# Optimization experiments

Hardware: AMD Instinct MI355X
Metric: run time of the kernel (lower is better)

The kernel has to match this reference:

```python
import jax, jax.numpy as jnp
import numpy as np

D_MODEL = 1024
N_HEADS = 16
D_HEAD = D_MODEL // N_HEADS
BSZ, SEQ = 1, 4096


def setup_inputs() -> dict:
    key = jax.random.key(0)
    ks = jax.random.split(key, 7)
    scale = 1.0 / np.sqrt(D_MODEL)
    q = jax.random.normal(ks[0], (BSZ, SEQ, D_MODEL), dtype=jnp.float32)
    k = jax.random.normal(ks[1], (BSZ, SEQ, D_MODEL), dtype=jnp.float32)
    v = jax.random.normal(ks[2], (BSZ, SEQ, D_MODEL), dtype=jnp.float32)
    Wq = jax.random.normal(ks[3], (D_MODEL, D_MODEL), dtype=jnp.float32) * scale
    Wk = jax.random.normal(ks[4], (D_MODEL, D_MODEL), dtype=jnp.float32) * scale
    Wv = jax.random.normal(ks[5], (D_MODEL, D_MODEL), dtype=jnp.float32) * scale
    Wo = jax.random.normal(ks[6], (D_MODEL, D_MODEL), dtype=jnp.float32) * scale
    # causal mask: 1 = attend, 0 = masked (matches torch masked_fill(mask == 0, -inf))
    mask = jnp.tril(jnp.ones((SEQ, SEQ), dtype=jnp.int32))[None, None, :, :]
    return {"q": q, "k": k, "v": v, "mask": mask, "Wq": Wq, "Wk": Wk, "Wv": Wv, "Wo": Wo}


def reference(q, k, v, mask, Wq, Wk, Wv, Wo):
    bsz, seq, _ = q.shape
    # nn.Linear(d,d,bias=False): y = x @ W.T
    Q = (q @ Wq.T).reshape(bsz, seq, N_HEADS, D_HEAD).transpose(0, 2, 1, 3)
    K = (k @ Wk.T).reshape(bsz, seq, N_HEADS, D_HEAD).transpose(0, 2, 1, 3)
    V = (v @ Wv.T).reshape(bsz, seq, N_HEADS, D_HEAD).transpose(0, 2, 1, 3)
    scores = jnp.einsum("bhqd,bhkd->bhqk", Q, K) / np.sqrt(D_HEAD).astype(np.float32)
    scores = jnp.where(mask == 0, -jnp.inf, scores)
    attn = jax.nn.softmax(scores, axis=-1)
    out = jnp.einsum("bhqk,bhkd->bhqd", attn, V)
    out = out.transpose(0, 2, 1, 3).reshape(bsz, seq, D_MODEL)
    return out @ Wo.T
```

## Files before the change

### kernel.cpp

```cpp
#include <hip/hip_runtime.h>


typedef __attribute__((ext_vector_type(8))) short bf16x8;
typedef __attribute__((ext_vector_type(4))) float f32x4;
typedef __attribute__((ext_vector_type(16))) float f32x16;

#define S_LEN 4096
#define DM 1024
#define NH 16
#define DH 64

static __device__ __forceinline__ unsigned short f2bf(float f) {
  union { float f; unsigned u; } x; x.f = f;
  unsigned u = x.u;
  u += 0x7fffu + ((u >> 16) & 1u);
  return (unsigned short)(u >> 16);
}

static __device__ __forceinline__ unsigned pk2(float lo, float hi) {
  unsigned r;
  asm("v_cvt_pk_bf16_f32 %0, %1, %2" : "=v"(r) : "v"(lo), "v"(hi));
  return r;
}

static __device__ __forceinline__ void swap32u(unsigned& a, unsigned& b) {
  asm("v_permlane32_swap_b32 %0, %1" : "+v"(a), "+v"(b));
}

static __device__ __forceinline__ float exp2_(float x) {
#if __has_builtin(__builtin_amdgcn_exp2f)
  return __builtin_amdgcn_exp2f(x);
#else
  return exp2f(x);
#endif
}

#define GLL16(gsrc, ldst)                                                      \
  __builtin_amdgcn_global_load_lds(                                            \
      (const __attribute__((address_space(1))) void*)(gsrc),                   \
      (__attribute__((address_space(3))) void*)(ldst), 16, 0, 0)

struct CastArgs {
  const float* src[8];
  unsigned short* dst[8];
  int n[8];
  float scl[8];
};

__global__ __launch_bounds__(256) void cast_all(CastArgs a) {
  int which = blockIdx.y;
  const float* __restrict__ src = a.src[which];
  unsigned short* __restrict__ dst = a.dst[which];
  int n = a.n[which];
  float s = a.scl[which];
  int i = (blockIdx.x * 256 + threadIdx.x) * 8;
  if (i >= n) return;
  f32x4 v0 = *(const f32x4*)(src + i);
  f32x4 v1 = *(const f32x4*)(src + i + 4);
  union { bf16x8 v; unsigned short u[8]; } o;
#pragma unroll
  for (int j = 0; j < 4; j++) { o.u[j] = f2bf(v0[j] * s); o.u[4 + j] = f2bf(v1[j] * s); }
  *(bf16x8*)(dst + i) = o.v;
}

static __device__ __forceinline__ void gemm_body(
    const unsigned short* __restrict__ A, const unsigned short* __restrict__ B,
    void* __restrict__ Cout, int mode, unsigned short* As, unsigned short* Bs) {
  const int K = 1024;
  int tid = threadIdx.x;
  int wid = tid >> 6, lane = tid & 63;
  int m0 = blockIdx.y * 128, n0 = blockIdx.x * 128;
  int wr = (wid >> 1) * 64, wc = (wid & 1) * 64;
  int g = lane >> 4, r = lane & 15;

  const int srow = wid * 8 + (lane >> 3);
  const int scol = 8 * ((lane & 7) ^ ((lane >> 3) & 7));
  const unsigned short* gA[4];
  const unsigned short* gB[4];
#pragma unroll
  for (int rr = 0; rr < 4; rr++) {
    gA[rr] = A + (size_t)(m0 + rr * 32 + srow) * K + scol;
    gB[rr] = B + (size_t)(n0 + rr * 32 + srow) * K + scol;
  }

  f32x4 acc[4][4] = {};
  const int rsw = (r & 7) << 3;

  for (int k0 = 0; k0 < K; k0 += 64) {
#pragma unroll
    for (int rr = 0; rr < 4; rr++) {
      GLL16(gA[rr] + k0, As + wid * 512 + rr * 2048);
      GLL16(gB[rr] + k0, Bs + wid * 512 + rr * 2048);
    }
    __syncthreads();

#pragma unroll
    for (int kk = 0; kk < 64; kk += 32) {
      bf16x8 af[4], bfr[4];
#pragma unroll
      for (int mi = 0; mi < 4; mi++)
        af[mi] = *(const bf16x8*)&As[(wr + mi * 16 + r) * 64 + ((kk + g * 8) ^ rsw)];
#pragma unroll
      for (int ni = 0; ni < 4; ni++)
        bfr[ni] = *(const bf16x8*)&Bs[(wc + ni * 16 + r) * 64 + ((kk + g * 8) ^ rsw)];
#pragma unroll
      for (int mi = 0; mi < 4; mi++)
#pragma unroll
        for (int ni = 0; ni < 4; ni++)
          acc[mi][ni] = __builtin_amdgcn_mfma_f32_16x16x32_bf16(
              af[mi], bfr[ni], acc[mi][ni], 0, 0, 0);
    }
    __syncthreads();
  }

  if (mode == 0) {
    float* C = (float*)Cout;
#pragma unroll
    for (int mi = 0; mi < 4; mi++) {
      int row = m0 + wr + mi * 16 + g * 4;
#pragma unroll
      for (int ni = 0; ni < 4; ni++) {
        int c = n0 + wc + ni * 16 + r;
#pragma unroll
        for (int j = 0; j < 4; j++)
          C[(size_t)(row + j) * DM + c] = acc[mi][ni][j];
      }
    }
  } else if (mode == 1) {
    unsigned short* Cb = (unsigned short*)Cout;
#pragma unroll
    for (int mi = 0; mi < 4; mi++) {
      int row = m0 + wr + mi * 16 + g * 4;
#pragma unroll
      for (int ni = 0; ni < 4; ni++) {
        int c = n0 + wc + ni * 16 + r;
        int h = c >> 6, d = c & 63;
#pragma unroll
        for (int j = 0; j < 4; j++)
          Cb[(size_t)h * (S_LEN * DH) + (size_t)(row + j) * DH + d] =
              f2bf(acc[mi][ni][j]);
      }
    }
  } else {
    unsigned short* Cb = (unsigned short*)Cout;
#pragma unroll
    for (int mi = 0; mi < 4; mi++) {
      int row = m0 + wr + mi * 16 + g * 4;
#pragma unroll
      for (int ni = 0; ni < 4; ni++) {
        int c = n0 + wc + ni * 16 + r;
        int h = c >> 6, d = c & 63;
#pragma unroll
        for (int j = 0; j < 4; j++) {
          int s = row + j;
          Cb[(size_t)h * (S_LEN * DH) + (size_t)(s >> 6) * 4096 + d * 64 + (s & 63)] =
              f2bf(acc[mi][ni][j]);
        }
      }
    }
  }
}

struct ProjArgs {
  const unsigned short* A[3];
  const unsigned short* B[3];
  unsigned short* C[3];
  int mode[3];
};

__global__ __launch_bounds__(256, 2) void gemm_proj(ProjArgs p) {
  __shared__ unsigned short As[8192];
  __shared__ unsigned short Bs[8192];
  int z = blockIdx.z;
  gemm_body(p.A[z], p.B[z], p.C[z], p.mode[z], As, Bs);
}

__global__ __launch_bounds__(256, 4) void gemm_one64(
    const unsigned short* __restrict__ A, const unsigned short* __restrict__ B,
    float* __restrict__ C) {
  __shared__ unsigned short As[4096];
  __shared__ unsigned short Bs[8192];
  const int K = 1024;
  int tid = threadIdx.x;
  int wid = tid >> 6, lane = tid & 63;
  int m0 = blockIdx.y * 64, n0 = blockIdx.x * 128;
  int wr = (wid >> 1) * 32, wc = (wid & 1) * 64;
  int g = lane >> 4, r = lane & 15;

  const int srow = wid * 8 + (lane >> 3);
  const int scol = 8 * ((lane & 7) ^ ((lane >> 3) & 7));
  const unsigned short* gA[2];
  const unsigned short* gB[4];
#pragma unroll
  for (int rr = 0; rr < 2; rr++)
    gA[rr] = A + (size_t)(m0 + rr * 32 + srow) * K + scol;
#pragma unroll
  for (int rr = 0; rr < 4; rr++)
    gB[rr] = B + (size_t)(n0 + rr * 32 + srow) * K + scol;

  f32x4 acc[2][4] = {};
  const int rsw = (r & 7) << 3;

  for (int k0 = 0; k0 < K; k0 += 64) {
#pragma unroll
    for (int rr = 0; rr < 2; rr++)
      GLL16(gA[rr] + k0, As + wid * 512 + rr * 2048);
#pragma unroll
    for (int rr = 0; rr < 4; rr++)
      GLL16(gB[rr] + k0, Bs + wid * 512 + rr * 2048);
    __syncthreads();

#pragma unroll
    for (int kk = 0; kk < 64; kk += 32) {
      bf16x8 af[2], bfr[4];
#pragma unroll
      for (int mi = 0; mi < 2; mi++)
        af[mi] = *(const bf16x8*)&As[(wr + mi * 16 + r) * 64 + ((kk + g * 8) ^ rsw)];
#pragma unroll
      for (int ni = 0; ni < 4; ni++)
        bfr[ni] = *(const bf16x8*)&Bs[(wc + ni * 16 + r) * 64 + ((kk + g * 8) ^ rsw)];
#pragma unroll
      for (int mi = 0; mi < 2; mi++)
#pragma unroll
        for (int ni = 0; ni < 4; ni++)
          acc[mi][ni] = __builtin_amdgcn_mfma_f32_16x16x32_bf16(
              af[mi], bfr[ni], acc[mi][ni], 0, 0, 0);
    }
    __syncthreads();
  }

#pragma unroll
  for (int mi = 0; mi < 2; mi++) {
    int row = m0 + wr + mi * 16 + g * 4;
#pragma unroll
    for (int ni = 0; ni < 4; ni++) {
      int c = n0 + wc + ni * 16 + r;
#pragma unroll
      for (int j = 0; j < 4; j++)
        C[(size_t)(row + j) * DM + c] = acc[mi][ni][j];
    }
  }
}

__global__ __launch_bounds__(512, 4) void attn_fwd(
    const unsigned short* __restrict__ Qh, const unsigned short* __restrict__ Kh,
    const unsigned short* __restrict__ V4, unsigned short* __restrict__ O) {
  __shared__ char smem[65536];

  const int b = blockIdx.x;
  const int hd = b & 15;
  const int t = b >> 4;
  const int qe = (t < 16) ? (31 - 2 * t) : (2 * (t - 16));
  const int q0 = qe * 128;
  const int nt = qe + 1;

  const int tid = threadIdx.x;
  const int gg = tid >> 8;
  const int ww = (tid >> 6) & 3;
  const int lane = tid & 63;
  const int l31 = lane & 31, hi = lane >> 5;
  const int qi = ww;
  const int qw = q0 + qi * 32;
  const int qrow = qw + l31;
  const int sw = (l31 & 7) << 4;

  const unsigned short* Qb = Qh + (size_t)hd * (S_LEN * DH);
  const char* Kb = (const char*)(Kh + (size_t)hd * (S_LEN * DH));
  const char* Vb = (const char*)(V4 + (size_t)hd * (S_LEN * DH));

  bf16x8 qf[4];
#pragma unroll
  for (int m = 0; m < 4; m++)
    qf[m] = *(const bf16x8*)&Qb[(size_t)qrow * DH + m * 16 + hi * 8];

  const int roleV = (ww >= 2);
  const int wv = ww & 1;
  const char* gb = roleV ? Vb : Kb;
  int soff[4];
#pragma unroll
  for (int q2 = 0; q2 < 4; q2++) {
    int rowl = wv * 32 + q2 * 8 + (lane >> 3);
    int cb = ((lane & 7) * 16) ^ (((lane >> 3) & 7) << 4);
    soff[q2] = rowl * 128 + cb;
  }
  const int ldsc = gg * 32768 + roleV * 8192 + wv * 4096;

  f32x16 oacc[2] = {};
  float m_r = 16.0f, l_r = 0.f;

  {
    const char* gp = gb + (long)(gg * nt) * 8192;
#pragma unroll
    for (int q2 = 0; q2 < 4; q2++)
      GLL16(gp + soff[q2], smem + ldsc + q2 * 1024);
  }
  __syncthreads();

  int db = 0;
  for (int it = 0; it < nt; ++it) {
    if (it + 1 < nt) {
      const char* gp = gb + (long)(gg * nt + it + 1) * 8192;
      char* lb = smem + ldsc + (db ^ 1) * 16384;
#pragma unroll
      for (int q2 = 0; q2 < 4; q2++)
        GLL16(gp + soff[q2], lb + q2 * 1024);
    }
    const int kv0 = (gg * nt + it) * 64;
    const char* Kc = smem + gg * 32768 + db * 16384;
    const char* Vc = Kc + 8192;

    if (kv0 <= qw + 31) {
      const bool hiP = (kv0 + 32 <= qw + 31);
      const bool interior = (kv0 + 63 <= qw);
      f32x16 s0 = {}, s1 = {};
#pragma unroll
      for (int m = 0; m < 4; m++) {
        bf16x8 kf = *(const bf16x8*)(Kc + l31 * 128 + ((m * 32 + hi * 16) ^ sw));
        s0 = __builtin_amdgcn_mfma_f32_32x32x16_bf16(kf, qf[m], s0, 0, 0, 0);
      }
      if (hiP) {
#pragma unroll
        for (int m = 0; m < 4; m++) {
          bf16x8 kf = *(const bf16x8*)(Kc + (32 + l31) * 128 + ((m * 32 + hi * 16) ^ sw));
          s1 = __builtin_amdgcn_mfma_f32_32x32x16_bf16(kf, qf[m], s1, 0, 0, 0);
        }
      }
      bf16x8 vf0[4];
#pragma unroll
      for (int i = 0; i < 4; i++) {
        const int dt = i >> 1, n = i & 1;
        vf0[i] = *(const bf16x8*)(Vc + (dt * 32 + l31) * 128 +
                   ((n * 32 + hi * 16) ^ sw));
      }
      if (!interior) {
#pragma unroll
        for (int rg = 0; rg < 16; rg++) {
          const int kvl = (rg & 3) + 8 * (rg >> 2) + 4 * hi;
          s0[rg] = (kv0 + kvl <= qrow) ? s0[rg] : -1e30f;
          s1[rg] = (hiP && kv0 + 32 + kvl <= qrow) ? s1[rg] : -1e30f;
        }
      }
#pragma unroll
      for (int rg = 0; rg < 16; rg++) {
        s0[rg] = exp2_(s0[rg] - m_r);
        s1[rg] = exp2_(s1[rg] - m_r);
      }
      float t0 = fmaxf(fmaxf(s0[0], s0[1]), s0[2]);
      float t1 = fmaxf(fmaxf(s0[3], s0[4]), s0[5]);
      float t2 = fmaxf(fmaxf(s0[6], s0[7]), s0[8]);
      float t3 = fmaxf(fmaxf(s0[9], s0[10]), s0[11]);
      float t4 = fmaxf(fmaxf(s0[12], s0[13]), s0[14]);
      float t5 = fmaxf(fmaxf(s0[15], s1[0]), s1[1]);
      float t6 = fmaxf(fmaxf(s1[2], s1[3]), s1[4]);
      float t7 = fmaxf(fmaxf(s1[5], s1[6]), s1[7]);
      float t8 = fmaxf(fmaxf(s1[8], s1[9]), s1[10]);
      float t9 = fmaxf(fmaxf(s1[11], s1[12]), s1[13]);
      float ta = fmaxf(s1[14], s1[15]);
      float u0 = fmaxf(fmaxf(t0, t1), t2);
      float u1 = fmaxf(fmaxf(t3, t4), t5);
      float u2 = fmaxf(fmaxf(t6, t7), t8);
      float u3 = fmaxf(t9, ta);
      float mxp = fmaxf(fmaxf(u0, u1), fmaxf(u2, u3));
      if (__any(mxp > 1024.0f)) {
        float mrow = fmaxf(mxp, __shfl_xor(mxp, 32, 64));
        float sc = 1.0f / mrow;
        m_r += __log2f(mrow);
        l_r *= sc;
#pragma unroll
        for (int rg = 0; rg < 16; rg++) { s0[rg] *= sc; s1[rg] *= sc; }
#pragma unroll
        for (int dt = 0; dt < 2; dt++)
#pragma unroll
          for (int rg = 0; rg < 16; rg++) oacc[dt][rg] *= sc;
      }
      float r0 = (s0[0] + s0[1]) + (s0[2] + s0[3]);
      float r1 = (s0[4] + s0[5]) + (s0[6] + s0[7]);
      float r2 = (s0[8] + s0[9]) + (s0[10] + s0[11]);
      float r3 = (s0[12] + s0[13]) + (s0[14] + s0[15]);
      float r4 = (s1[0] + s1[1]) + (s1[2] + s1[3]);
      float r5 = (s1[4] + s1[5]) + (s1[6] + s1[7]);
      float r6 = (s1[8] + s1[9]) + (s1[10] + s1[11]);
      float r7 = (s1[12] + s1[13]) + (s1[14] + s1[15]);
      float rs = ((r0 + r1) + (r2 + r3)) + ((r4 + r5) + (r6 + r7));
      l_r += rs;
#pragma unroll
      for (int c = 0; c < 2; c++) {
        if (c == 0 || hiP) {
          const f32x16 P = c ? s1 : s0;
#pragma unroll
          for (int n = 0; n < 2; n++) {
            unsigned a0 = pk2(P[8 * n + 0], P[8 * n + 1]);
            unsigned a1 = pk2(P[8 * n + 2], P[8 * n + 3]);
            unsigned b0 = pk2(P[8 * n + 4], P[8 * n + 5]);
            unsigned b1 = pk2(P[8 * n + 6], P[8 * n + 7]);
            swap32u(a0, b0);
            swap32u(a1, b1);
            union { unsigned w[4]; bf16x8 v; } u;
            u.w[0] = a0; u.w[1] = a1; u.w[2] = b0; u.w[3] = b1;
#pragma unroll
            for (int dt = 0; dt < 2; dt++) {
              bf16x8 vf = (c == 0) ? vf0[dt * 2 + n]
                        : *(const bf16x8*)(Vc + (dt * 32 + l31) * 128 +
                             ((64 + n * 32 + hi * 16) ^ sw));
              oacc[dt] = __builtin_amdgcn_mfma_f32_32x32x16_bf16(
                  vf, u.v, oacc[dt], 0, 0, 0);
            }
          }
        }
      }
    }
    __syncthreads();
    db ^= 1;
  }

  l_r += __shfl_xor(l_r, 32, 64);

  float* scr = (float*)smem;
  const int sbase = (qi * 64 + lane) * 35;
  if (gg == 1) {
#pragma unroll
    for (int dt = 0; dt < 2; dt++)
#pragma unroll
      for (int rg = 0; rg < 16; rg++) scr[sbase + dt * 16 + rg] = oacc[dt][rg];
    scr[sbase + 32] = m_r;
    scr[sbase + 33] = l_r;
  }
  __syncthreads();
  if (gg == 0) {
    float mB = scr[sbase + 32], lB = scr[sbase + 33];
    float mS = fmaxf(m_r, mB);
    float sA = exp2_(m_r - mS);
    float sB = exp2_(mB - mS);
    float rl = 1.0f / (l_r * sA + lB * sB);
    float fA = sA * rl, fB = sB * rl;
#pragma unroll
    for (int dt = 0; dt < 2; dt++)
#pragma unroll
      for (int blk = 0; blk < 4; blk++) {
        float v0 = oacc[dt][blk * 4 + 0] * fA + scr[sbase + dt * 16 + blk * 4 + 0] * fB;
        float v1 = oacc[dt][blk * 4 + 1] * fA + scr[sbase + dt * 16 + blk * 4 + 1] * fB;
        float v2 = oacc[dt][blk * 4 + 2] * fA + scr[sbase + dt * 16 + blk * 4 + 2] * fB;
        float v3 = oacc[dt][blk * 4 + 3] * fA + scr[sbase + dt * 16 + blk * 4 + 3] * fB;
        uint2 st; st.x = pk2(v0, v1); st.y = pk2(v2, v3);
        int d0 = dt * 32 + blk * 8 + 4 * hi;
        *(uint2*)&O[(size_t)qrow * DM + hd * DH + d0] = st;
      }
  }
}

extern "C" void kernel_launch(void* const* d_in, const int* in_sizes, int n_in,
                              void* d_out, int out_size, void* d_ws, size_t ws_size,
                              hipStream_t stream) {
  const float* q = (const float*)d_in[0];
  const float* k = (const float*)d_in[1];
  const float* v = (const float*)d_in[2];
  const float* Wq = (const float*)d_in[4];
  const float* Wk = (const float*)d_in[5];
  const float* Wv = (const float*)d_in[6];
  const float* Wo = (const float*)d_in[7];

  unsigned short* W = (unsigned short*)d_ws;
  const int SM = S_LEN * DM;
  const int WM = DM * DM;
  unsigned short* qb  = W;
  unsigned short* kb  = qb + SM;
  unsigned short* vb  = kb + SM;
  unsigned short* Wqb = vb + SM;
  unsigned short* Wkb = Wqb + WM;
  unsigned short* Wvb = Wkb + WM;
  unsigned short* Wob = Wvb + WM;
  unsigned short* Qh  = Wob + WM;
  unsigned short* Kh  = Qh + SM;
  unsigned short* V4  = Kh + SM;
  unsigned short* Ob  = V4 + SM;

  CastArgs ca;
  ca.src[0] = q;  ca.dst[0] = qb;  ca.n[0] = SM; ca.scl[0] = 1.f;
  ca.src[1] = k;  ca.dst[1] = kb;  ca.n[1] = SM; ca.scl[1] = 1.f;
  ca.src[2] = v;  ca.dst[2] = vb;  ca.n[2] = SM; ca.scl[2] = 1.f;
  ca.src[3] = Wq; ca.dst[3] = Wqb; ca.n[3] = WM; ca.scl[3] = 0.125f * 1.44269504f;
  ca.src[4] = Wk; ca.dst[4] = Wkb; ca.n[4] = WM; ca.scl[4] = 1.f;
  ca.src[5] = Wv; ca.dst[5] = Wvb; ca.n[5] = WM; ca.scl[5] = 1.f;
  ca.src[6] = Wo; ca.dst[6] = Wob; ca.n[6] = WM; ca.scl[6] = 1.f;
  ca.src[7] = Wo; ca.dst[7] = Wob; ca.n[7] = 0;  ca.scl[7] = 1.f;
  cast_all<<<dim3(2048, 8), 256, 0, stream>>>(ca);

  ProjArgs pa;
  pa.A[0] = qb; pa.B[0] = Wqb; pa.C[0] = Qh; pa.mode[0] = 1;
  pa.A[1] = kb; pa.B[1] = Wkb; pa.C[1] = Kh; pa.mode[1] = 1;
  pa.A[2] = vb; pa.B[2] = Wvb; pa.C[2] = V4; pa.mode[2] = 2;
  gemm_proj<<<dim3(8, 32, 3), 256, 0, stream>>>(pa);

  attn_fwd<<<dim3(512), 512, 0, stream>>>(Qh, Kh, V4, Ob);

  gemm_one64<<<dim3(8, 64), 256, 0, stream>>>(Ob, Wob, (float*)d_out);
}
```

Baseline: 122.9 us.

## Fuse fp32-to-bf16 activation cast into projection GEMM A-tile loads

Drops the separate cast of q/k/v to bf16. The projection GEMM now reads fp32 activations directly into registers, packs them to bf16 with v_cvt_pk_bf16_f32 and stores them into the swizzled LDS tile, while B still goes through global_load_lds. This removes writing and re-reading three bf16 activation copies, but each GEMM block now reads fp32 A tiles (twice the bytes), once per column block. The A loads are also synchronous register loads rather than async LDS loads.

```diff
diff --git a/kernel.cpp b/kernel.cpp
--- a/kernel.cpp
+++ b/kernel.cpp
@@ -41,20 +41,17 @@
       (__attribute__((address_space(3))) void*)(ldst), 16, 0, 0)
 
 struct CastArgs {
-  const float* src[8];
-  unsigned short* dst[8];
-  int n[8];
-  float scl[8];
+  const float* src[4];
+  unsigned short* dst[4];
+  float scl[4];
 };
 
 __global__ __launch_bounds__(256) void cast_all(CastArgs a) {
   int which = blockIdx.y;
   const float* __restrict__ src = a.src[which];
   unsigned short* __restrict__ dst = a.dst[which];
-  int n = a.n[which];
   float s = a.scl[which];
   int i = (blockIdx.x * 256 + threadIdx.x) * 8;
-  if (i >= n) return;
   f32x4 v0 = *(const f32x4*)(src + i);
   f32x4 v1 = *(const f32x4*)(src + i + 4);
   union { bf16x8 v; unsigned short u[8]; } o;
@@ -63,9 +60,10 @@
   *(bf16x8*)(dst + i) = o.v;
 }
 
-static __device__ __forceinline__ void gemm_body(
-    const unsigned short* __restrict__ A, const unsigned short* __restrict__ B,
-    void* __restrict__ Cout, int mode, unsigned short* As, unsigned short* Bs) {
+static __device__ __forceinline__ void gemm_bodyF(
+    const float* __restrict__ Af, const unsigned short* __restrict__ B,
+    unsigned short* __restrict__ Cb, int mode, unsigned short* As,
+    unsigned short* Bs) {
   const int K = 1024;
   int tid = threadIdx.x;
   int wid = tid >> 6, lane = tid & 63;
@@ -75,11 +73,11 @@
 
   const int srow = wid * 8 + (lane >> 3);
   const int scol = 8 * ((lane & 7) ^ ((lane >> 3) & 7));
-  const unsigned short* gA[4];
+  const float* gA[4];
   const unsigned short* gB[4];
 #pragma unroll
   for (int rr = 0; rr < 4; rr++) {
-    gA[rr] = A + (size_t)(m0 + rr * 32 + srow) * K + scol;
+    gA[rr] = Af + (size_t)(m0 + rr * 32 + srow) * K + scol;
     gB[rr] = B + (size_t)(n0 + rr * 32 + srow) * K + scol;
   }
 
@@ -88,9 +86,22 @@
 
   for (int k0 = 0; k0 < K; k0 += 64) {
 #pragma unroll
+    for (int rr = 0; rr < 4; rr++)
+      GLL16(gB[rr] + k0, Bs + wid * 512 + rr * 2048);
+    f32x4 a0[4], a1[4];
+#pragma unroll
     for (int rr = 0; rr < 4; rr++) {
-      GLL16(gA[rr] + k0, As + wid * 512 + rr * 2048);
-      GLL16(gB[rr] + k0, Bs + wid * 512 + rr * 2048);
+      a0[rr] = *(const f32x4*)(gA[rr] + k0);
+      a1[rr] = *(const f32x4*)(gA[rr] + k0 + 4);
+    }
+#pragma unroll
+    for (int rr = 0; rr < 4; rr++) {
+      union { unsigned w[4]; bf16x8 v; } pkv;
+      pkv.w[0] = pk2(a0[rr][0], a0[rr][1]);
+      pkv.w[1] = pk2(a0[rr][2], a0[rr][3]);
+      pkv.w[2] = pk2(a1[rr][0], a1[rr][1]);
+      pkv.w[3] = pk2(a1[rr][2], a1[rr][3]);
+      *(bf16x8*)(As + wid * 512 + rr * 2048 + lane * 8) = pkv.v;
     }
     __syncthreads();
 
@@ -113,21 +124,7 @@
     __syncthreads();
   }
 
-  if (mode == 0) {
-    float* C = (float*)Cout;
-#pragma unroll
-    for (int mi = 0; mi < 4; mi++) {
-      int row = m0 + wr + mi * 16 + g * 4;
-#pragma unroll
-      for (int ni = 0; ni < 4; ni++) {
-        int c = n0 + wc + ni * 16 + r;
-#pragma unroll
-        for (int j = 0; j < 4; j++)
-          C[(size_t)(row + j) * DM + c] = acc[mi][ni][j];
-      }
-    }
-  } else if (mode == 1) {
-    unsigned short* Cb = (unsigned short*)Cout;
+  if (mode == 1) {
 #pragma unroll
     for (int mi = 0; mi < 4; mi++) {
       int row = m0 + wr + mi * 16 + g * 4;
@@ -142,7 +139,6 @@
       }
     }
   } else {
-    unsigned short* Cb = (unsigned short*)Cout;
 #pragma unroll
     for (int mi = 0; mi < 4; mi++) {
       int row = m0 + wr + mi * 16 + g * 4;
@@ -161,18 +157,18 @@
   }
 }
 
-struct ProjArgs {
-  const unsigned short* A[3];
+struct ProjArgsF {
+  const float* A[3];
   const unsigned short* B[3];
   unsigned short* C[3];
   int mode[3];
 };
 
-__global__ __launch_bounds__(256, 2) void gemm_proj(ProjArgs p) {
+__global__ __launch_bounds__(256, 2) void gemm_projF(ProjArgsF p) {
   __shared__ unsigned short As[8192];
   __shared__ unsigned short Bs[8192];
   int z = blockIdx.z;
-  gemm_body(p.A[z], p.B[z], p.C[z], p.mode[z], As, Bs);
+  gemm_bodyF(p.A[z], p.B[z], p.C[z], p.mode[z], As, Bs);
 }
 
 __global__ __launch_bounds__(256, 4) void gemm_one64(
@@ -462,10 +458,7 @@
   unsigned short* W = (unsigned short*)d_ws;
   const int SM = S_LEN * DM;
   const int WM = DM * DM;
-  unsigned short* qb  = W;
-  unsigned short* kb  = qb + SM;
-  unsigned short* vb  = kb + SM;
-  unsigned short* Wqb = vb + SM;
+  unsigned short* Wqb = W;
   unsigned short* Wkb = Wqb + WM;
   unsigned short* Wvb = Wkb + WM;
   unsigned short* Wob = Wvb + WM;
@@ -475,21 +468,17 @@
   unsigned short* Ob  = V4 + SM;
 
   CastArgs ca;
-  ca.src[0] = q;  ca.dst[0] = qb;  ca.n[0] = SM; ca.scl[0] = 1.f;
-  ca.src[1] = k;  ca.dst[1] = kb;  ca.n[1] = SM; ca.scl[1] = 1.f;
-  ca.src[2] = v;  ca.dst[2] = vb;  ca.n[2] = SM; ca.scl[2] = 1.f;
-  ca.src[3] = Wq; ca.dst[3] = Wqb; ca.n[3] = WM; ca.scl[3] = 0.125f * 1.44269504f;
-  ca.src[4] = Wk; ca.dst[4] = Wkb; ca.n[4] = WM; ca.scl[4] = 1.f;
-  ca.src[5] = Wv; ca.dst[5] = Wvb; ca.n[5] = WM; ca.scl[5] = 1.f;
-  ca.src[6] = Wo; ca.dst[6] = Wob; ca.n[6] = WM; ca.scl[6] = 1.f;
-  ca.src[7] = Wo; ca.dst[7] = Wob; ca.n[7] = 0;  ca.scl[7] = 1.f;
-  cast_all<<<dim3(2048, 8), 256, 0, stream>>>(ca);
-
-  ProjArgs pa;
-  pa.A[0] = qb; pa.B[0] = Wqb; pa.C[0] = Qh; pa.mode[0] = 1;
-  pa.A[1] = kb; pa.B[1] = Wkb; pa.C[1] = Kh; pa.mode[1] = 1;
-  pa.A[2] = vb; pa.B[2] = Wvb; pa.C[2] = V4; pa.mode[2] = 2;
-  gemm_proj<<<dim3(8, 32, 3), 256, 0, stream>>>(pa);
+  ca.src[0] = Wq; ca.dst[0] = Wqb; ca.scl[0] = 0.125f * 1.44269504f;
+  ca.src[1] = Wk; ca.dst[1] = Wkb; ca.scl[1] = 1.f;
+  ca.src[2] = Wv; ca.dst[2] = Wvb; ca.scl[2] = 1.f;
+  ca.src[3] = Wo; ca.dst[3] = Wob; ca.scl[3] = 1.f;
+  cast_all<<<dim3(512, 4), 256, 0, stream>>>(ca);
+
+  ProjArgsF pa;
+  pa.A[0] = q; pa.B[0] = Wqb; pa.C[0] = Qh; pa.mode[0] = 1;
+  pa.A[1] = k; pa.B[1] = Wkb; pa.C[1] = Kh; pa.mode[1] = 1;
+  pa.A[2] = v; pa.B[2] = Wvb; pa.C[2] = V4; pa.mode[2] = 2;
+  gemm_projF<<<dim3(8, 32, 3), 256, 0, stream>>>(pa);
 
   attn_fwd<<<dim3(512), 512, 0, stream>>>(Qh, Kh, V4, Ob);
 
```

Result: slower. 140.0 us (+14.0%).
